# Kernel optimization log

Measured on AMD Instinct MI355X. Metric: run time of the kernel, lower is better.

The kernel has to match this reference:

```python
import jax, jax.numpy as jnp
import numpy as np

K = 20
EPS = 1e-5   # BatchNorm eps (eval mode: running_mean=0, running_var=1)
SLOPE = 0.2


def knn_idx(x, k):
    # x: [B,F,N] -> idx [B,N,k]; top-k of negative squared distance (includes self)
    xx = jnp.sum(x * x, axis=1)                       # [B,N]
    inner = jnp.einsum('bfn,bfm->bnm', x, x)          # [B,N,N]
    neg_d = 2.0 * inner - xx[:, :, None] - xx[:, None, :]
    _, idx = jax.lax.top_k(neg_d, k)
    return idx


def gather_neighbors(x_nt, idx):
    # x_nt [B,N,F], idx [B,N,k] -> [B,N,k,F]
    return jax.vmap(lambda xt, ix: xt[ix])(x_nt, idx)


def group_layer(x_bfn, idx):
    # GroupLayer: [B,F,N] -> [B,2F,N,k] = cat(neigh - center, neigh)
    x_nt = jnp.transpose(x_bfn, (0, 2, 1))
    neigh = gather_neighbors(x_nt, idx)
    feat = jnp.concatenate([neigh - x_nt[:, :, None, :], neigh], axis=-1)
    return jnp.transpose(feat, (0, 3, 1, 2))


def eigen_graph(pts_bfn, k):
    # pts_bfn [B,3,N] -> feature [B,15,N], idx_EU [B,N,k], idx_EI [B,N,k]
    B, _, N = pts_bfn.shape
    idx_eu = knn_idx(pts_bfn, k)
    pts_nt = jnp.transpose(pts_bfn, (0, 2, 1))        # [B,N,3]
    neigh = gather_neighbors(pts_nt, idx_eu)          # [B,N,k,3]
    diff = neigh - pts_nt[:, :, None, :]
    cov = jnp.einsum('bnki,bnkj->bnij', diff, diff)   # [B,N,3,3] symmetric PSD
    eigval, eigvec = jnp.linalg.eigh(cov)             # [B,N,3], [B,N,3,3]
    feature = jnp.concatenate([pts_nt, eigval, eigvec.reshape(B, N, 9)], axis=2)
    idx_ei = knn_idx(jnp.transpose(eigval, (0, 2, 1)), k)
    return jnp.transpose(feature, (0, 2, 1)), idx_eu, idx_ei


def first_group_layer(x_bfn, idx_eu, idx_ei):
    # x_bfn [B,15,N]: [:,0:3]=xyz, [:,3:6]=eigenvalues -> [B,12,N,k]
    xyz = jnp.transpose(x_bfn[:, 0:3, :], (0, 2, 1))
    eig = jnp.transpose(x_bfn[:, 3:6, :], (0, 2, 1))
    nx = gather_neighbors(xyz, idx_eu)
    gx = jnp.concatenate([nx - xyz[:, :, None, :], nx], axis=-1)
    ne = gather_neighbors(eig, idx_ei)
    ge = jnp.concatenate([ne - eig[:, :, None, :], ne], axis=-1)
    out = jnp.concatenate([gx, ge], axis=-1)
    return jnp.transpose(out, (0, 3, 1, 2))


def graph_distance(pts_bfn, idx):
    pts_nt = jnp.transpose(pts_bfn, (0, 2, 1))
    d = gather_neighbors(pts_nt, idx) - pts_nt[:, :, None, :]
    s = jnp.sum(d * d, axis=-1)
    return jnp.sqrt(jnp.maximum(s, 1e-12))[:, None, :, :]  # [B,1,N,k]


def conv_bn_lrelu(x, w, g, b):
    # 1x1 conv (no bias) + eval-mode BN + LeakyReLU(0.2)
    if x.ndim == 4:
        y = jnp.einsum('oc,bcnk->bonk', w, x)
        g_, b_ = g[None, :, None, None], b[None, :, None, None]
    else:
        y = jnp.einsum('oc,bcn->bon', w, x)
        g_, b_ = g[None, :, None], b[None, :, None]
    y = y / jnp.sqrt(1.0 + EPS) * g_ + b_
    return jax.nn.leaky_relu(y, SLOPE)


def fps(points, n_samples):
    # furthest point sampling, start at index 0. points [B,N,3] -> [B,S] int32
    B, N, _ = points.shape
    init = jnp.zeros((B,), jnp.int32)
    dist0 = jnp.full((B, N), 1e10, points.dtype)

    def body(carry, _):
        dist, last = carry
        lastp = jnp.take_along_axis(points, last[:, None, None].astype(jnp.int32), axis=1)
        d = jnp.sum((points - lastp) ** 2, axis=-1)
        dist = jnp.minimum(dist, d)
        nxt = jnp.argmax(dist, axis=-1).astype(jnp.int32)
        return (dist, nxt), nxt

    (_, _), rest = jax.lax.scan(body, (dist0, init), None, length=n_samples - 1)
    return jnp.concatenate([init[None, :], rest], axis=0).T


def gather_op(x_bcn, idx):
    # x [B,C,N], idx [B,S] -> [B,C,S]
    return jnp.take_along_axis(x_bcn, idx[:, None, :], axis=2)


def forward(x, conv1_w, bn1_g, bn1_b, conv2_w, bn2_g, bn2_b, conv3_w, bn3_g, bn3_b,
            conv5_w, bn5_g, bn5_b, lin1_w, bn6_g, bn6_b, lin2_w, lin2_b,
            bn7_g, bn7_b, lin3_w, lin3_b):
    B, _, N1 = x.shape
    N2, N3 = N1 // 2, N1 // 4
    pts1 = jnp.transpose(x, (0, 2, 1))  # [B,N,3]

    # GSCM layer 1 (first layer)
    feat, idx_eu, idx_ei = eigen_graph(x, K)
    g = first_group_layer(feat, idx_eu, idx_ei)            # [B,12,N1,K]
    g = jnp.concatenate([g, graph_distance(x, idx_eu)], axis=1)  # [B,13,N1,K]
    x1 = conv_bn_lrelu(g, conv1_w, bn1_g, bn1_b).max(axis=-1)     # [B,64,N1]

    # downsample to N2
    id2 = fps(pts1, N2)
    pts2_bfn = gather_op(x, id2)                            # [B,3,N2]
    x1_ds = gather_op(x1, id2)                              # [B,64,N2]

    # GSCM layer 2
    _, idx_eu2, idx_ei2 = eigen_graph(pts2_bfn, K)
    g2 = jnp.concatenate([group_layer(x1_ds, idx_eu2), group_layer(x1_ds, idx_ei2)], axis=1)
    x2 = conv_bn_lrelu(g2, conv2_w, bn2_g, bn2_b).max(axis=-1)    # [B,64,N2]

    # downsample to N3
    pts2_nt = jnp.transpose(pts2_bfn, (0, 2, 1))
    id3 = fps(pts2_nt, N3)
    pts3_bfn = gather_op(pts2_bfn, id3)
    x2_ds = gather_op(x2, id3)
    x1_ds = gather_op(x1_ds, id3)

    # GSCM layer 3
    _, idx_eu3, idx_ei3 = eigen_graph(pts3_bfn, K)
    g3 = jnp.concatenate([group_layer(x2_ds, idx_eu3), group_layer(x2_ds, idx_ei3)], axis=1)
    x3 = conv_bn_lrelu(g3, conv3_w, bn3_g, bn3_b).max(axis=-1)    # [B,128,N3]

    h = jnp.concatenate([x1_ds, x2_ds, x3], axis=1)        # [B,256,N3]
    h = conv_bn_lrelu(h, conv5_w, bn5_g, bn5_b)            # [B,emb,N3]
    h = jnp.concatenate([h.max(axis=-1), h.mean(axis=-1)], axis=1)  # [B,2*emb]

    y = jnp.einsum('oi,bi->bo', lin1_w, h)
    y = jax.nn.leaky_relu(y / jnp.sqrt(1.0 + EPS) * bn6_g + bn6_b, SLOPE)
    y = jnp.einsum('oi,bi->bo', lin2_w, y) + lin2_b
    y = jax.nn.leaky_relu(y / jnp.sqrt(1.0 + EPS) * bn7_g + bn7_b, SLOPE)
    return jnp.einsum('oi,bi->bo', lin3_w, y) + lin3_b     # [B,40]


def setup_inputs() -> dict:
    key = jax.random.key(0)
    ks = jax.random.split(key, 10)
    B, N, EMB, OUT = 16, 1024, 1024, 40

    def w(k_, o, i):
        return jax.random.normal(k_, (o, i), jnp.float32) * (1.0 / np.sqrt(i))

    return {
        'x': jax.random.normal(ks[0], (B, 3, N), jnp.float32),
        'conv1_w': w(ks[1], 64, 13), 'bn1_g': jnp.ones((64,)), 'bn1_b': jnp.zeros((64,)),
        'conv2_w': w(ks[2], 64, 256), 'bn2_g': jnp.ones((64,)), 'bn2_b': jnp.zeros((64,)),
        'conv3_w': w(ks[3], 128, 256), 'bn3_g': jnp.ones((128,)), 'bn3_b': jnp.zeros((128,)),
        'conv5_w': w(ks[4], EMB, 256), 'bn5_g': jnp.ones((EMB,)), 'bn5_b': jnp.zeros((EMB,)),
        'lin1_w': w(ks[5], 512, 2 * EMB), 'bn6_g': jnp.ones((512,)), 'bn6_b': jnp.zeros((512,)),
        'lin2_w': w(ks[6], 256, 512), 'lin2_b': jnp.zeros((256,)),
        'bn7_g': jnp.ones((256,)), 'bn7_b': jnp.zeros((256,)),
        'lin3_w': w(ks[7], OUT, 256), 'lin3_b': jnp.zeros((OUT,)),
    }


def reference(x, conv1_w, bn1_g, bn1_b, conv2_w, bn2_g, bn2_b, conv3_w, bn3_g, bn3_b,
              conv5_w, bn5_g, bn5_b, lin1_w, bn6_g, bn6_b, lin2_w, lin2_b,
              bn7_g, bn7_b, lin3_w, lin3_b):
    return forward(x, conv1_w, bn1_g, bn1_b, conv2_w, bn2_g, bn2_b, conv3_w, bn3_g, bn3_b,
                   conv5_w, bn5_g, bn5_b, lin1_w, bn6_g, bn6_b, lin2_w, lin2_b,
                   bn7_g, bn7_b, lin3_w, lin3_b)
```

## Files before the change

### kernel.cpp

```cpp
#include <hip/hip_runtime.h>
#include <math.h>

#define KNB 20
constexpr float BN_INV = 0.9999950000374997f;
constexpr float SLOPE = 0.2f;

__device__ __forceinline__ float lrelu(float v){ return v >= 0.f ? v : SLOPE*v; }

__global__ __launch_bounds__(256) void prep_kernel(const float* __restrict__ x, float* __restrict__ pts,
                            const float* __restrict__ conv2w, float* __restrict__ Wc2,
                            const float* __restrict__ conv3w, float* __restrict__ Wc3){
  int i = blockIdx.x*256 + threadIdx.x;
  if (i < 16*1024){
    int b = i >> 10, n = i & 1023;
    const float* xb = x + (size_t)b*3*1024;
    float* p = pts + (size_t)i*3;
    p[0]=xb[n]; p[1]=xb[1024+n]; p[2]=xb[2048+n];
  } else if (i < 16*1024 + 64*64){
    int e = i - 16*1024;
    int o = e >> 6, c = e & 63;
    float wa=conv2w[(size_t)o*256+c], wb=conv2w[(size_t)o*256+64+c];
    float wc=conv2w[(size_t)o*256+128+c], wd=conv2w[(size_t)o*256+192+c];
    Wc2[((size_t)0*64+o)*64+c]=wa+wb; Wc2[((size_t)1*64+o)*64+c]=wc+wd; Wc2[((size_t)2*64+o)*64+c]=wa+wc;
  } else if (i < 16*1024 + 64*64 + 128*64){
    int e = i - 16*1024 - 64*64;
    int o = e >> 6, c = e & 63;
    float wa=conv3w[(size_t)o*256+c], wb=conv3w[(size_t)o*256+64+c];
    float wc=conv3w[(size_t)o*256+128+c], wd=conv3w[(size_t)o*256+192+c];
    Wc3[((size_t)0*128+o)*64+c]=wa+wb; Wc3[((size_t)1*128+o)*64+c]=wc+wd; Wc3[((size_t)2*128+o)*64+c]=wa+wc;
  }
}

template<int N, bool TOGLOBAL>
__device__ void knn_core(const float* __restrict__ pts, int* __restrict__ idx_global,
                         int* __restrict__ sOut, int chunk, int b, float4* sp){
#pragma clang fp contract(off)
  constexpr int E = N/64;
  int t = threadIdx.x;
  const float* pb = pts + (size_t)b*N*3;
  for (int e = t; e < N; e += 256){
    float x0=pb[e*3], x1=pb[e*3+1], x2=pb[e*3+2];
    sp[e] = make_float4(x0, x1, x2, (x0*x0 + x1*x1) + x2*x2);
  }
  __syncthreads();
  int wave = t >> 6, lane = t & 63;
  int row = chunk*4 + wave;
  float4 P = sp[row];
  float nd[E];
  #pragma unroll
  for (int i=0;i<E;++i){
    float4 Q = sp[lane + i*64];
    float inner = (P.x*Q.x + P.y*Q.y) + P.z*Q.z;
    nd[i] = (2.0f*inner - P.w) - Q.w;
  }
  int myout = 0;
  for (int j=0;j<KNB;++j){
    float bv = nd[0]; int bi = lane;
    #pragma unroll
    for (int i=1;i<E;++i){
      if (nd[i] > bv){ bv = nd[i]; bi = lane + i*64; }
    }
    #pragma unroll
    for (int off=1; off<64; off<<=1){
      float ov = __shfl_xor(bv, off);
      int oi = __shfl_xor(bi, off);
      if (ov > bv || (ov == bv && oi < bi)){ bv = ov; bi = oi; }
    }
    if (lane == j) myout = bi;
    if (lane == (bi & 63)){
      int slot = bi >> 6;
      #pragma unroll
      for (int i=0;i<E;++i) if (i == slot) nd[i] = -INFINITY;
    }
  }
  if (TOGLOBAL){
    if (lane < KNB) idx_global[((size_t)b*N + row)*KNB + lane] = myout;
  } else {
    if (lane < KNB) sOut[lane] = myout;
  }
}

template<int N>
__global__ __launch_bounds__(256) void knn_kernel(const float* __restrict__ pts, int* __restrict__ idx){
  __shared__ float4 sp[N];
  knn_core<N,true>(pts, idx, nullptr, blockIdx.x, blockIdx.y, sp);
}

#define DECLQ4(i) float4 Q##i = sp[(i)*256 + tid]; float D##i = 1e10f; \
  asm volatile("" : "+v"(Q##i.x), "+v"(Q##i.y), "+v"(Q##i.z));
#define UPD4(i, B) { float dx=Q##i.x-L.x; float dy=Q##i.y-L.y; float dz=Q##i.z-L.z; \
  float dd=fminf(D##i,(dx*dx+dy*dy)+dz*dz); D##i=dd; \
  unsigned long long k=((unsigned long long)__float_as_uint(dd)<<32)|(unsigned long long)(nl-(unsigned)((i)*256)); \
  if(k>B)B=k; }
#define DPPMAX(ctrl) { unsigned lo=(unsigned)bk, hi=(unsigned)(bk>>32); \
  unsigned lo2=(unsigned)__builtin_amdgcn_mov_dpp((int)lo, ctrl, 0xF, 0xF, true); \
  unsigned hi2=(unsigned)__builtin_amdgcn_mov_dpp((int)hi, ctrl, 0xF, 0xF, true); \
  unsigned long long ok=((unsigned long long)hi2<<32)|lo2; if(ok>bk)bk=ok; }
#define FPS_STEP_TAIL \
      DPPMAX(0xB1) DPPMAX(0x4E) DPPMAX(0x124) DPPMAX(0x128) DPPMAX(0x142) DPPMAX(0x143) \
      if (lane == 63) rk[((s&1)<<2) | w] = bk; \
      __syncthreads(); \
      { const unsigned long long* rp = rk + ((s&1)<<2); \
        unsigned long long k0=rp[0], k1=rp[1], k2=rp[2], k3=rp[3]; \
        unsigned long long km1 = k0>k1?k0:k1, km2 = k2>k3?k2:k3; \
        unsigned long long kk = km1>km2?km1:km2; \
        last = (int)(~(unsigned int)kk); } \
      if (tid==0) idout[(size_t)b*M + s] = last;

template<int N, int M>
__device__ void fps_body4(const float* __restrict__ pts, int* __restrict__ idout,
                          int b, float4* sp, unsigned long long* rk){
#pragma clang fp contract(off)
  constexpr int E4 = N/256;
  int tid = threadIdx.x;
  const float* pb = pts + (size_t)b*N*3;
  for (int e=tid; e<N; e+=256){
    sp[e] = make_float4(pb[e*3], pb[e*3+1], pb[e*3+2], 0.f);
  }
  __syncthreads();
  __builtin_amdgcn_s_setprio(1);
  int lane = tid & 63, w = tid >> 6;
  unsigned int nl = ~(unsigned int)tid;
  int last = 0;
  if (tid==0) idout[(size_t)b*M] = 0;
  if constexpr (E4 == 4){
    DECLQ4(0) DECLQ4(1) DECLQ4(2) DECLQ4(3)
    for (int s=1; s<M; ++s){
      float4 L = sp[last];
      unsigned long long b0=0ULL,b1=0ULL,b2=0ULL,b3=0ULL;
      UPD4(0,b0) UPD4(1,b1) UPD4(2,b2) UPD4(3,b3)
      unsigned long long kl_ = b0>b1?b0:b1, kh_ = b2>b3?b2:b3;
      unsigned long long bk = kl_>kh_?kl_:kh_;
      FPS_STEP_TAIL
    }
  } else {
    DECLQ4(0) DECLQ4(1)
    for (int s=1; s<M; ++s){
      float4 L = sp[last];
      unsigned long long b0=0ULL,b1=0ULL;
      UPD4(0,b0) UPD4(1,b1)
      unsigned long long bk = b0>b1?b0:b1;
      FPS_STEP_TAIL
    }
  }
}

template<int N>
__global__ void cov_eig_kernel(const float* __restrict__ pts, const int* __restrict__ idx,
                               float* __restrict__ eigval){
  int i = blockIdx.x*blockDim.x + threadIdx.x;
  if (i >= 16*N) return;
  int b = i / N, n = i % N;
  const float* pb = pts + (size_t)b*N*3;
  const int* ix = idx + (size_t)i*KNB;
  float cx = pb[n*3], cy = pb[n*3+1], cz = pb[n*3+2];
  float c00=0,c01=0,c02=0,c11=0,c12=0,c22=0;
  for (int k=0;k<KNB;++k){
    int m = ix[k];
    float dx = pb[m*3]-cx, dy = pb[m*3+1]-cy, dz = pb[m*3+2]-cz;
    c00 += dx*dx; c01 += dx*dy; c02 += dx*dz;
    c11 += dy*dy; c12 += dy*dz; c22 += dz*dz;
  }
  double a00=c00,a01=c01,a02=c02,a11=c11,a12=c12,a22=c22;
  double p1 = a01*a01 + a02*a02 + a12*a12;
  double q = (a00+a11+a22)/3.0;
  double b00=a00-q, b11=a11-q, b22=a22-q;
  double p2 = b00*b00+b11*b11+b22*b22 + 2.0*p1;
  double e0,e1,e2;
  if (p2 <= 0.0){
    e0=e1=e2=q;
  } else {
    double p = sqrt(p2/6.0);
    double det = b00*(b11*b22 - a12*a12) - a01*(a01*b22 - a12*a02) + a02*(a01*a12 - b11*a02);
    double r = det / (2.0*p*p*p);
    r = fmin(1.0, fmax(-1.0, r));
    double phi = acos(r)/3.0;
    double big = q + 2.0*p*cos(phi);
    double sml = q + 2.0*p*cos(phi + 2.0943951023931953);
    double mid = 3.0*q - big - sml;
    e0 = sml; e1 = mid; e2 = big;
  }
  float* ev = eigval + (size_t)i*3;
  ev[0]=(float)e0; ev[1]=(float)e1; ev[2]=(float)e2;
}

__device__ void stage1_body(
    const float* __restrict__ eig, const float* __restrict__ pts,
    const int* __restrict__ idx_eu,
    const float* __restrict__ w, const float* __restrict__ g, const float* __restrict__ bb,
    float* __restrict__ x1, int chunk, int b,
    float4* sp, int (*sIei)[KNB], float (*feat)[13][KNB]){
  constexpr int N = 1024;
  int t = threadIdx.x, wave = t>>6, lane = t&63;
  knn_core<N,false>(eig, nullptr, &sIei[wave][0], chunk, b, sp);
  int row = chunk*4 + wave;
  size_t i = (size_t)b*N + row;
  const float* pb = pts + (size_t)b*N*3;
  if (lane < KNB){
    int ieu = idx_eu[i*KNB + lane];
    int iei = sIei[wave][lane];
    float4 ne4 = sp[iei];
    float4 ee4 = sp[row];
    float d2 = 0.f;
    #pragma unroll
    for (int f=0; f<3; ++f){
      float nx = pb[ieu*3+f], xx = pb[row*3+f];
      float dfv = nx - xx;
      feat[wave][f][lane] = dfv; feat[wave][3+f][lane] = nx;
      float ne = (f==0)? ne4.x : ((f==1)? ne4.y : ne4.z);
      float ee = (f==0)? ee4.x : ((f==1)? ee4.y : ee4.z);
      feat[wave][6+f][lane] = ne - ee; feat[wave][9+f][lane] = ne;
      d2 += dfv*dfv;
    }
    feat[wave][12][lane] = sqrtf(fmaxf(d2, 1e-12f));
  }
  __syncthreads();
  float wr[13];
  #pragma unroll
  for (int c=0;c<13;++c) wr[c] = w[lane*13+c];
  float sg = BN_INV * g[lane], sb = bb[lane];
  float mx = -INFINITY;
  for (int k=0;k<KNB;++k){
    float s = 0.f;
    #pragma unroll
    for (int c=0;c<13;++c) s = fmaf(wr[c], feat[wave][c][k], s);
    mx = fmaxf(mx, lrelu(fmaf(s, sg, sb)));
  }
  x1[i*64 + lane] = mx;
}

__global__ __launch_bounds__(256, 1) void mega1_kernel(
    const float* __restrict__ pts1, int* __restrict__ fps_id,
    const float* __restrict__ eig1, const int* __restrict__ idx_eu,
    const float* __restrict__ w, const float* __restrict__ g, const float* __restrict__ bb,
    float* __restrict__ x1){
  __shared__ float4 sp[1024];
  __shared__ int sIei[4][KNB];
  __shared__ float feat[4][13][KNB];
  __shared__ unsigned long long rk[8];
  if (blockIdx.x < 16){
    fps_body4<1024,512>(pts1, fps_id, blockIdx.x, sp, rk);
  } else {
    int bx = blockIdx.x - 16;
    stage1_body(eig1, pts1, idx_eu, w, g, bb, x1, bx & 255, bx >> 8, sp, sIei, feat);
  }
}

template<int COUT, int N>
__device__ void gm_body(const float* __restrict__ eig,
    const float* __restrict__ PQR, int Mtot,
    const int* __restrict__ idx_eu,
    const float* __restrict__ g, const float* __restrict__ bb,
    float* __restrict__ xout, int chunk, int b, float4* sp, int* sIeiW){
  int t = threadIdx.x, wave = t>>6, lane = t&63;
  knn_core<N,false>(eig, nullptr, sIeiW, chunk, b, sp);
  __syncthreads();
  int row = chunk*4 + wave;
  size_t i = (size_t)b*N + row;
  const float* P = PQR;
  const float* Q = PQR + (size_t)Mtot*COUT;
  const float* R = PQR + (size_t)2*Mtot*COUT;
  for (int o = lane; o < COUT; o += 64){
    float base = R[i*COUT + o];
    float sg = BN_INV*g[o], sb = bb[o];
    float mx = -INFINITY;
    for (int k=0;k<KNB;++k){
      int eu = idx_eu[i*KNB + k];
      int ei = sIeiW[k];
      float v = P[((size_t)b*N + eu)*COUT + o] + Q[((size_t)b*N + ei)*COUT + o] - base;
      mx = fmaxf(mx, lrelu(fmaf(v, sg, sb)));
    }
    xout[i*COUT + o] = mx;
  }
}

template<int COUT, int N>
__global__ __launch_bounds__(256) void knn_ei_gm_kernel(
    const float* __restrict__ eig, const float* __restrict__ PQR, int Mtot,
    const int* __restrict__ idx_eu, const float* __restrict__ g, const float* __restrict__ bb,
    float* __restrict__ xout){
  __shared__ float4 sp[N];
  __shared__ int sIei[4][KNB];
  int wave = threadIdx.x >> 6;
  gm_body<COUT,N>(eig, PQR, Mtot, idx_eu, g, bb, xout, blockIdx.x, blockIdx.y, sp, &sIei[wave][0]);
}

template<int COUT, int N, int M>
__global__ __launch_bounds__(256, 1) void gmfps_kernel(
    const float* __restrict__ eig, const float* __restrict__ ptsN,
    const float* __restrict__ PQR, int Mtot,
    const int* __restrict__ idx_eu, const float* __restrict__ g, const float* __restrict__ bb,
    float* __restrict__ xout, int* __restrict__ fps_id){
  __shared__ float4 sp[N];
  __shared__ int sIei[4][KNB];
  __shared__ unsigned long long rk[8];
  if (blockIdx.x < 16){
    fps_body4<N,M>(ptsN, fps_id, blockIdx.x, sp, rk);
    return;
  }
  int bx = blockIdx.x - 16;
  int wave = threadIdx.x >> 6;
  gm_body<COUT,N>(eig, PQR, Mtot, idx_eu, g, bb, xout, bx % (N/4), bx / (N/4), sp, &sIei[wave][0]);
}

__global__ __launch_bounds__(256) void gather2_kernel(const float* __restrict__ pts1, const float* __restrict__ x1,
                               const int* __restrict__ id2, float* __restrict__ pts2, float* __restrict__ x1d){
  int i = blockIdx.x*256 + threadIdx.x;
  if (i < 16*512){
    int b = i >> 9;
    int src = id2[i];
    const float* p = pts1 + ((size_t)b*1024 + src)*3;
    float* o = pts2 + (size_t)i*3;
    o[0]=p[0]; o[1]=p[1]; o[2]=p[2];
  } else {
    int e = i - 16*512;
    if (e < 16*512*64){
      int c = e & 63, r = e >> 6;
      int b = r >> 9, s = r & 511;
      int src = id2[(size_t)b*512 + s];
      x1d[e] = x1[((size_t)b*1024 + src)*64 + c];
    }
  }
}

__global__ __launch_bounds__(256) void gather3_kernel(const float* __restrict__ pts2, const float* __restrict__ x2,
                               const float* __restrict__ x1d, const int* __restrict__ id3,
                               float* __restrict__ pts3, float* __restrict__ x2d, float* __restrict__ x1dd){
  int i = blockIdx.x*256 + threadIdx.x;
  if (i < 16*256){
    int b = i >> 8;
    int src = id3[i];
    const float* p = pts2 + ((size_t)b*512 + src)*3;
    float* o = pts3 + (size_t)i*3;
    o[0]=p[0]; o[1]=p[1]; o[2]=p[2];
  } else {
    int e = i - 16*256;
    if (e < 16*256*64){
      int c = e & 63, r = e >> 6;
      int b = r >> 8, s = r & 255;
      int src = id3[(size_t)b*256 + s];
      x2d[e] = x2[((size_t)b*512 + src)*64 + c];
    } else {
      int e2 = e - 16*256*64;
      if (e2 < 16*256*64){
        int c = e2 & 63, r = e2 >> 6;
        int b = r >> 8, s = r & 255;
        int src = id3[(size_t)b*256 + s];
        x1dd[e2] = x1d[((size_t)b*512 + src)*64 + c];
      }
    }
  }
}

template<int COUT>
__global__ __launch_bounds__(256) void gemm_xw_kernel(
    const float* __restrict__ X, const float* __restrict__ Wc,
    float* __restrict__ PQR, int Mtot){
  __shared__ float sA[64][68];
  __shared__ float sW[64][68];
  int mt = blockIdx.x, ot = blockIdx.y, set = blockIdx.z;
  int t = threadIdx.x;
  for (int e=t; e<4096; e+=256){ int r=e>>6, c=e&63; sA[r][c] = X[(size_t)(mt*64+r)*64 + c]; }
  const float* Wp = Wc + ((size_t)set*COUT + ot*64)*64;
  for (int e=t; e<4096; e+=256){ int r=e>>6, c=e&63; sW[r][c] = Wp[(size_t)r*64 + c]; }
  __syncthreads();
  int tx = t & 15, ty = t >> 4;
  float acc[4][4];
  #pragma unroll
  for (int r=0;r<4;++r)
    #pragma unroll
    for (int j=0;j<4;++j) acc[r][j]=0.f;
  #pragma unroll
  for (int k4=0;k4<16;++k4){
    float4 A0 = *(const float4*)&sA[ty*4+0][k4*4];
    float4 A1 = *(const float4*)&sA[ty*4+1][k4*4];
    float4 A2 = *(const float4*)&sA[ty*4+2][k4*4];
    float4 A3 = *(const float4*)&sA[ty*4+3][k4*4];
    float4 W0 = *(const float4*)&sW[tx*4+0][k4*4];
    float4 W1 = *(const float4*)&sW[tx*4+1][k4*4];
    float4 W2 = *(const float4*)&sW[tx*4+2][k4*4];
    float4 W3 = *(const float4*)&sW[tx*4+3][k4*4];
    float4 A[4] = {A0,A1,A2,A3};
    float4 W[4] = {W0,W1,W2,W3};
    #pragma unroll
    for (int r=0;r<4;++r)
      #pragma unroll
      for (int j=0;j<4;++j){
        float s = acc[r][j];
        s = fmaf(A[r].x, W[j].x, s);
        s = fmaf(A[r].y, W[j].y, s);
        s = fmaf(A[r].z, W[j].z, s);
        s = fmaf(A[r].w, W[j].w, s);
        acc[r][j] = s;
      }
  }
  float* outp = PQR + (size_t)set*Mtot*COUT;
  #pragma unroll
  for (int r=0;r<4;++r){
    float4 v = make_float4(acc[r][0], acc[r][1], acc[r][2], acc[r][3]);
    *(float4*)&outp[(size_t)(mt*64 + ty*4 + r)*COUT + ot*64 + tx*4] = v;
  }
}

__global__ __launch_bounds__(256) void conv5_gemm_kernel(
    const float* __restrict__ x1dd, const float* __restrict__ x2d, const float* __restrict__ x3,
    const float* __restrict__ w, const float* __restrict__ g, const float* __restrict__ bb,
    float* __restrict__ pmax, float* __restrict__ psum){
  __shared__ float sA[64][68];
  __shared__ float sB[64][68];
  int otile = blockIdx.x, ntile = blockIdx.y, b = blockIdx.z;
  int t = threadIdx.x;
  int tx = t & 15, ty = t >> 4;
  float acc[4][4];
  #pragma unroll
  for (int i=0;i<4;++i)
    #pragma unroll
    for (int j=0;j<4;++j) acc[i][j] = 0.f;
  for (int kc=0; kc<4; ++kc){
    #pragma unroll 4
    for (int e = t; e < 4096; e += 256){
      int nl = e >> 6, kl = e & 63;
      int n = ntile*64 + nl;
      float v;
      if (kc == 0)      v = x1dd[((size_t)b*256 + n)*64 + kl];
      else if (kc == 1) v = x2d [((size_t)b*256 + n)*64 + kl];
      else              v = x3  [((size_t)b*256 + n)*128 + (kc-2)*64 + kl];
      sA[nl][kl] = v;
    }
    #pragma unroll 4
    for (int e = t; e < 4096; e += 256){
      int ol = e >> 6, kl = e & 63;
      sB[ol][kl] = w[((size_t)(otile*64 + ol))*256 + kc*64 + kl];
    }
    __syncthreads();
    #pragma unroll
    for (int k4=0; k4<16; ++k4){
      float4 a0 = *(const float4*)&sA[ty*4+0][k4*4];
      float4 a1 = *(const float4*)&sA[ty*4+1][k4*4];
      float4 a2 = *(const float4*)&sA[ty*4+2][k4*4];
      float4 a3 = *(const float4*)&sA[ty*4+3][k4*4];
      float4 b0 = *(const float4*)&sB[tx*4+0][k4*4];
      float4 b1 = *(const float4*)&sB[tx*4+1][k4*4];
      float4 b2 = *(const float4*)&sB[tx*4+2][k4*4];
      float4 b3 = *(const float4*)&sB[tx*4+3][k4*4];
      float4 A[4] = {a0,a1,a2,a3};
      float4 Bv[4] = {b0,b1,b2,b3};
      #pragma unroll
      for (int i=0;i<4;++i)
        #pragma unroll
        for (int j=0;j<4;++j){
          float s = acc[i][j];
          s = fmaf(A[i].x, Bv[j].x, s);
          s = fmaf(A[i].y, Bv[j].y, s);
          s = fmaf(A[i].z, Bv[j].z, s);
          s = fmaf(A[i].w, Bv[j].w, s);
          acc[i][j] = s;
        }
    }
    __syncthreads();
  }
  float sg[4], sbv[4];
  #pragma unroll
  for (int j=0;j<4;++j){
    int o = otile*64 + tx*4 + j;
    sg[j] = BN_INV*g[o]; sbv[j] = bb[o];
  }
  float mx[4], sm[4];
  #pragma unroll
  for (int j=0;j<4;++j){ mx[j]=-INFINITY; sm[j]=0.f; }
  #pragma unroll
  for (int i=0;i<4;++i)
    #pragma unroll
    for (int j=0;j<4;++j){
      float vv = lrelu(fmaf(acc[i][j], sg[j], sbv[j]));
      mx[j] = fmaxf(mx[j], vv);
      sm[j] += vv;
    }
  float* redM = &sA[0][0];
  float* redS = redM + 16*64;
  #pragma unroll
  for (int j=0;j<4;++j){
    redM[ty*64 + tx*4 + j] = mx[j];
    redS[ty*64 + tx*4 + j] = sm[j];
  }
  __syncthreads();
  if (t < 64){
    float m = -INFINITY, s = 0.f;
    #pragma unroll
    for (int r=0;r<16;++r){
      m = fmaxf(m, redM[r*64 + t]);
      s += redS[r*64 + t];
    }
    int o = otile*64 + t;
    pmax[((size_t)b*1024 + o)*4 + ntile] = m;
    psum[((size_t)b*1024 + o)*4 + ntile] = s;
  }
}

__global__ __launch_bounds__(256) void lin1_kernel(const float* __restrict__ pmax, const float* __restrict__ psum,
    const float* __restrict__ w, const float* __restrict__ g, const float* __restrict__ bb,
    float* __restrict__ y1){
  __shared__ float sh[2048];
  int b = blockIdx.y; int o = blockIdx.x*256 + threadIdx.x;
  for (int e=threadIdx.x; e<2048; e+=256){
    if (e < 1024){
      const float* pm = pmax + ((size_t)b*1024 + e)*4;
      sh[e] = fmaxf(fmaxf(pm[0],pm[1]), fmaxf(pm[2],pm[3]));
    } else {
      const float* ps = psum + ((size_t)b*1024 + (e-1024))*4;
      sh[e] = ((ps[0]+ps[1])+(ps[2]+ps[3])) * (1.0f/256.0f);
    }
  }
  __syncthreads();
  const float* wr = w + (size_t)o*2048;
  float acc=0.f;
  for (int c=0;c<2048;++c) acc = fmaf(wr[c], sh[c], acc);
  y1[(size_t)b*512+o] = lrelu(fmaf(acc, BN_INV*g[o], bb[o]));
}

__global__ __launch_bounds__(256) void lin23_kernel(const float* __restrict__ y1,
    const float* __restrict__ w2, const float* __restrict__ lb2,
    const float* __restrict__ g, const float* __restrict__ bb,
    const float* __restrict__ w3, const float* __restrict__ lb3,
    float* __restrict__ outp){
  __shared__ float sh1[512];
  __shared__ float sh2[256];
  int b = blockIdx.x; int o = threadIdx.x;
  for (int e=o; e<512; e+=256) sh1[e]=y1[(size_t)b*512+e];
  __syncthreads();
  {
    const float* wr = w2 + (size_t)o*512;
    float acc=0.f;
    for (int c=0;c<512;++c) acc = fmaf(wr[c], sh1[c], acc);
    acc += lb2[o];
    sh2[o] = lrelu(fmaf(acc, BN_INV*g[o], bb[o]));
  }
  __syncthreads();
  if (o < 40){
    const float* wr = w3 + (size_t)o*256;
    float acc=0.f;
    for (int c=0;c<256;++c) acc = fmaf(wr[c], sh2[c], acc);
    outp[(size_t)b*40+o] = acc + lb3[o];
  }
}

extern "C" void kernel_launch(void* const* d_in, const int* in_sizes, int n_in,
                              void* d_out, int out_size, void* d_ws, size_t ws_size,
                              hipStream_t stream) {
  const float* x      = (const float*)d_in[0];
  const float* conv1w = (const float*)d_in[1];
  const float* bn1g   = (const float*)d_in[2];
  const float* bn1b   = (const float*)d_in[3];
  const float* conv2w = (const float*)d_in[4];
  const float* bn2g   = (const float*)d_in[5];
  const float* bn2b   = (const float*)d_in[6];
  const float* conv3w = (const float*)d_in[7];
  const float* bn3g   = (const float*)d_in[8];
  const float* bn3b   = (const float*)d_in[9];
  const float* conv5w = (const float*)d_in[10];
  const float* bn5g   = (const float*)d_in[11];
  const float* bn5b   = (const float*)d_in[12];
  const float* lin1w  = (const float*)d_in[13];
  const float* bn6g   = (const float*)d_in[14];
  const float* bn6b   = (const float*)d_in[15];
  const float* lin2w  = (const float*)d_in[16];
  const float* lin2b  = (const float*)d_in[17];
  const float* bn7g   = (const float*)d_in[18];
  const float* bn7b   = (const float*)d_in[19];
  const float* lin3w  = (const float*)d_in[20];
  const float* lin3b  = (const float*)d_in[21];
  float* outp = (float*)d_out;

  char* ws = (char*)d_ws;
  size_t off = 0;
  auto alloc = [&](size_t bytes)->char*{
    off = (off + 255) & ~(size_t)255;
    char* p = ws + off; off += bytes; return p;
  };
  const int B=16, N1=1024, N2=512, N3=256;
  float* pts1 = (float*)alloc((size_t)B*N1*3*4);
  int*   ieu1 = (int*)alloc((size_t)B*N1*KNB*4);
  float* eig1 = (float*)alloc((size_t)B*N1*3*4);
  float* x1   = (float*)alloc((size_t)B*N1*64*4);
  int*   id2  = (int*)alloc((size_t)B*N2*4);
  float* pts2 = (float*)alloc((size_t)B*N2*3*4);
  float* x1d  = (float*)alloc((size_t)B*N2*64*4);
  int*   ieu2 = (int*)alloc((size_t)B*N2*KNB*4);
  float* eig2 = (float*)alloc((size_t)B*N2*3*4);
  float* x2   = (float*)alloc((size_t)B*N2*64*4);
  int*   id3  = (int*)alloc((size_t)B*N3*4);
  float* pts3 = (float*)alloc((size_t)B*N3*3*4);
  float* x2d  = (float*)alloc((size_t)B*N3*64*4);
  float* x1dd = (float*)alloc((size_t)B*N3*64*4);
  int*   ieu3 = (int*)alloc((size_t)B*N3*KNB*4);
  float* eig3 = (float*)alloc((size_t)B*N3*3*4);
  float* x3   = (float*)alloc((size_t)B*N3*128*4);
  float* pmax = (float*)alloc((size_t)B*1024*4*4);
  float* psum = (float*)alloc((size_t)B*1024*4*4);
  float* y1   = (float*)alloc((size_t)B*512*4);
  float* Wc2  = (float*)alloc((size_t)3*64*64*4);
  float* Wc3  = (float*)alloc((size_t)3*128*64*4);
  float* PQR2 = (float*)alloc((size_t)3*B*N2*64*4);
  float* PQR3 = (float*)alloc((size_t)3*B*N3*128*4);

  prep_kernel<<<112, 256, 0, stream>>>(x, pts1, conv2w, Wc2, conv3w, Wc3);
  knn_kernel<1024><<<dim3(256,16), 256, 0, stream>>>(pts1, ieu1);
  cov_eig_kernel<1024><<<(B*N1+255)/256, 256, 0, stream>>>(pts1, ieu1, eig1);
  mega1_kernel<<<16 + 4096, 256, 0, stream>>>(pts1, id2, eig1, ieu1, conv1w, bn1g, bn1b, x1);
  gather2_kernel<<<2080, 256, 0, stream>>>(pts1, x1, id2, pts2, x1d);
  knn_kernel<512><<<dim3(128,16), 256, 0, stream>>>(pts2, ieu2);
  cov_eig_kernel<512><<<(B*N2+255)/256, 256, 0, stream>>>(pts2, ieu2, eig2);
  gemm_xw_kernel<64><<<dim3(B*N2/64, 1, 3), 256, 0, stream>>>(x1d, Wc2, PQR2, B*N2);
  gmfps_kernel<64,512,256><<<16 + 2048, 256, 0, stream>>>(eig2, pts2, PQR2, B*N2, ieu2, bn2g, bn2b, x2, id3);
  gather3_kernel<<<2064, 256, 0, stream>>>(pts2, x2, x1d, id3, pts3, x2d, x1dd);
  knn_kernel<256><<<dim3(64,16), 256, 0, stream>>>(pts3, ieu3);
  cov_eig_kernel<256><<<(B*N3+255)/256, 256, 0, stream>>>(pts3, ieu3, eig3);
  gemm_xw_kernel<128><<<dim3(B*N3/64, 2, 3), 256, 0, stream>>>(x2d, Wc3, PQR3, B*N3);
  knn_ei_gm_kernel<128,256><<<dim3(64,16), 256, 0, stream>>>(eig3, PQR3, B*N3, ieu3, bn3g, bn3b, x3);
  conv5_gemm_kernel<<<dim3(16,4,16), 256, 0, stream>>>(x1dd, x2d, x3, conv5w, bn5g, bn5b, pmax, psum);
  lin1_kernel<<<dim3(2,16), 256, 0, stream>>>(pmax, psum, lin1w, bn6g, bn6b, y1);
  lin23_kernel<<<16, 256, 0, stream>>>(y1, lin2w, lin2b, bn7g, bn7b, lin3w, lin3b, outp);
}
```

Baseline: 602.1 us.

## Fuse kNN with covariance eigen solve and merge independent GEMM launches

Merges the kNN and covariance-eigenvalue kernels: each block now handles several rows per wave, keeps the indices in shared memory and computes eigenvalues from the shared point cache, so the index re-read and one launch go away. At stages 2 and 3 the independent X·W GEMM blocks are folded into the same launch as the kNN/cov blocks, cutting launches and letting the two workloads run side by side. The costs are more rows per block and higher shared-memory use, since both GEMM tiles and the point cache are allocated in every block, which can lower occupancy. The eigen step now runs on only 4×RPW threads per block, which serialises it.

```diff
diff --git a/kernel.cpp b/kernel.cpp
--- a/kernel.cpp
+++ b/kernel.cpp
@@ -31,11 +31,44 @@
   }
 }
 
+template<int N>
+__device__ int knn_row(const float4* sp, int row, int lane){
+#pragma clang fp contract(off)
+  constexpr int E = N/64;
+  float4 P = sp[row];
+  float nd[E];
+  #pragma unroll
+  for (int i=0;i<E;++i){
+    float4 Q = sp[lane + i*64];
+    float inner = (P.x*Q.x + P.y*Q.y) + P.z*Q.z;
+    nd[i] = (2.0f*inner - P.w) - Q.w;
+  }
+  int myout = 0;
+  for (int j=0;j<KNB;++j){
+    float bv = nd[0]; int bi = lane;
+    #pragma unroll
+    for (int i=1;i<E;++i){
+      if (nd[i] > bv){ bv = nd[i]; bi = lane + i*64; }
+    }
+    #pragma unroll
+    for (int off=1; off<64; off<<=1){
+      float ov = __shfl_xor(bv, off);
+      int oi = __shfl_xor(bi, off);
+      if (ov > bv || (ov == bv && oi < bi)){ bv = ov; bi = oi; }
+    }
+    if (lane == j) myout = bi;
+    if (lane == (bi & 63)){
+      int slot = bi >> 6;
+      #pragma unroll
+      for (int i=0;i<E;++i) if (i == slot) nd[i] = -INFINITY;
+    }
+  }
+  return myout;
+}
+
 template<int N, bool TOGLOBAL>
 __device__ void knn_core(const float* __restrict__ pts, int* __restrict__ idx_global,
                          int* __restrict__ sOut, int chunk, int b, float4* sp){
-#pragma clang fp contract(off)
-  constexpr int E = N/64;
   int t = threadIdx.x;
   const float* pb = pts + (size_t)b*N*3;
   for (int e = t; e < N; e += 256){
@@ -45,34 +78,7 @@
   __syncthreads();
   int wave = t >> 6, lane = t & 63;
   int row = chunk*4 + wave;
-  float4 P = sp[row];
-  float nd[E];
-  #pragma unroll
-  for (int i=0;i<E;++i){
-    float4 Q = sp[lane + i*64];
-    float inner = (P.x*Q.x + P.y*Q.y) + P.z*Q.z;
-    nd[i] = (2.0f*inner - P.w) - Q.w;
-  }
-  int myout = 0;
-  for (int j=0;j<KNB;++j){
-    float bv = nd[0]; int bi = lane;
-    #pragma unroll
-    for (int i=1;i<E;++i){
-      if (nd[i] > bv){ bv = nd[i]; bi = lane + i*64; }
-    }
-    #pragma unroll
-    for (int off=1; off<64; off<<=1){
-      float ov = __shfl_xor(bv, off);
-      int oi = __shfl_xor(bi, off);
-      if (ov > bv || (ov == bv && oi < bi)){ bv = ov; bi = oi; }
-    }
-    if (lane == j) myout = bi;
-    if (lane == (bi & 63)){
-      int slot = bi >> 6;
-      #pragma unroll
-      for (int i=0;i<E;++i) if (i == slot) nd[i] = -INFINITY;
-    }
-  }
+  int myout = knn_row<N>(sp, row, lane);
   if (TOGLOBAL){
     if (lane < KNB) idx_global[((size_t)b*N + row)*KNB + lane] = myout;
   } else {
@@ -80,10 +86,73 @@
   }
 }
 
-template<int N>
-__global__ __launch_bounds__(256) void knn_kernel(const float* __restrict__ pts, int* __restrict__ idx){
+__device__ void cov_eig_row(const float4* sp, const int* sIdxRow, int row, float* ev){
+  float cx = sp[row].x, cy = sp[row].y, cz = sp[row].z;
+  float c00=0,c01=0,c02=0,c11=0,c12=0,c22=0;
+  for (int k=0;k<KNB;++k){
+    int m = sIdxRow[k];
+    float dx = sp[m].x-cx, dy = sp[m].y-cy, dz = sp[m].z-cz;
+    c00 += dx*dx; c01 += dx*dy; c02 += dx*dz;
+    c11 += dy*dy; c12 += dy*dz; c22 += dz*dz;
+  }
+  double a00=c00,a01=c01,a02=c02,a11=c11,a12=c12,a22=c22;
+  double p1 = a01*a01 + a02*a02 + a12*a12;
+  double q = (a00+a11+a22)/3.0;
+  double b00=a00-q, b11=a11-q, b22=a22-q;
+  double p2 = b00*b00+b11*b11+b22*b22 + 2.0*p1;
+  double e0,e1,e2;
+  if (p2 <= 0.0){
+    e0=e1=e2=q;
+  } else {
+    double p = sqrt(p2/6.0);
+    double det = b00*(b11*b22 - a12*a12) - a01*(a01*b22 - a12*a02) + a02*(a01*a12 - b11*a02);
+    double r = det / (2.0*p*p*p);
+    r = fmin(1.0, fmax(-1.0, r));
+    double phi = acos(r)/3.0;
+    double big = q + 2.0*p*cos(phi);
+    double sml = q + 2.0*p*cos(phi + 2.0943951023931953);
+    double mid = 3.0*q - big - sml;
+    e0 = sml; e1 = mid; e2 = big;
+  }
+  ev[0]=(float)e0; ev[1]=(float)e1; ev[2]=(float)e2;
+}
+
+template<int N, int RPW>
+__device__ void knn_cov_body(const float* __restrict__ pts, int* __restrict__ idx,
+                             float* __restrict__ eigval, int cb, int b,
+                             float4* sp, int (*sIdx)[KNB]){
+  constexpr int ROWS = 4*RPW;
+  int t = threadIdx.x;
+  const float* pb = pts + (size_t)b*N*3;
+  for (int e = t; e < N; e += 256){
+    float x0=pb[e*3], x1=pb[e*3+1], x2=pb[e*3+2];
+    sp[e] = make_float4(x0, x1, x2, (x0*x0 + x1*x1) + x2*x2);
+  }
+  __syncthreads();
+  int wave = t >> 6, lane = t & 63;
+  #pragma unroll
+  for (int r=0; r<RPW; ++r){
+    int lr = wave*RPW + r;
+    int row = cb*ROWS + lr;
+    int myout = knn_row<N>(sp, row, lane);
+    if (lane < KNB){
+      sIdx[lr][lane] = myout;
+      idx[((size_t)b*N + row)*KNB + lane] = myout;
+    }
+  }
+  __syncthreads();
+  if (t < ROWS){
+    int row = cb*ROWS + t;
+    cov_eig_row(sp, &sIdx[t][0], row, eigval + ((size_t)b*N + row)*3);
+  }
+}
+
+template<int N, int RPW>
+__global__ __launch_bounds__(256) void knn_cov_kernel(const float* __restrict__ pts,
+    int* __restrict__ idx, float* __restrict__ eigval){
   __shared__ float4 sp[N];
-  knn_core<N,true>(pts, idx, nullptr, blockIdx.x, blockIdx.y, sp);
+  __shared__ int sIdx[4*RPW][KNB];
+  knn_cov_body<N,RPW>(pts, idx, eigval, blockIdx.x, blockIdx.y, sp, sIdx);
 }
 
 #define DECLQ4(i) float4 Q##i = sp[(i)*256 + tid]; float D##i = 1e10f; \
@@ -145,45 +214,6 @@
   }
 }
 
-template<int N>
-__global__ void cov_eig_kernel(const float* __restrict__ pts, const int* __restrict__ idx,
-                               float* __restrict__ eigval){
-  int i = blockIdx.x*blockDim.x + threadIdx.x;
-  if (i >= 16*N) return;
-  int b = i / N, n = i % N;
-  const float* pb = pts + (size_t)b*N*3;
-  const int* ix = idx + (size_t)i*KNB;
-  float cx = pb[n*3], cy = pb[n*3+1], cz = pb[n*3+2];
-  float c00=0,c01=0,c02=0,c11=0,c12=0,c22=0;
-  for (int k=0;k<KNB;++k){
-    int m = ix[k];
-    float dx = pb[m*3]-cx, dy = pb[m*3+1]-cy, dz = pb[m*3+2]-cz;
-    c00 += dx*dx; c01 += dx*dy; c02 += dx*dz;
-    c11 += dy*dy; c12 += dy*dz; c22 += dz*dz;
-  }
-  double a00=c00,a01=c01,a02=c02,a11=c11,a12=c12,a22=c22;
-  double p1 = a01*a01 + a02*a02 + a12*a12;
-  double q = (a00+a11+a22)/3.0;
-  double b00=a00-q, b11=a11-q, b22=a22-q;
-  double p2 = b00*b00+b11*b11+b22*b22 + 2.0*p1;
-  double e0,e1,e2;
-  if (p2 <= 0.0){
-    e0=e1=e2=q;
-  } else {
-    double p = sqrt(p2/6.0);
-    double det = b00*(b11*b22 - a12*a12) - a01*(a01*b22 - a12*a02) + a02*(a01*a12 - b11*a02);
-    double r = det / (2.0*p*p*p);
-    r = fmin(1.0, fmax(-1.0, r));
-    double phi = acos(r)/3.0;
-    double big = q + 2.0*p*cos(phi);
-    double sml = q + 2.0*p*cos(phi + 2.0943951023931953);
-    double mid = 3.0*q - big - sml;
-    e0 = sml; e1 = mid; e2 = big;
-  }
-  float* ev = eigval + (size_t)i*3;
-  ev[0]=(float)e0; ev[1]=(float)e1; ev[2]=(float)e2;
-}
-
 __device__ void stage1_body(
     const float* __restrict__ eig, const float* __restrict__ pts,
     const int* __restrict__ idx_eu,
@@ -303,6 +333,86 @@
   gm_body<COUT,N>(eig, PQR, Mtot, idx_eu, g, bb, xout, bx % (N/4), bx / (N/4), sp, &sIei[wave][0]);
 }
 
+template<int COUT>
+__device__ void gemm_xw_body(const float* __restrict__ X, const float* __restrict__ Wc,
+    float* __restrict__ PQR, int Mtot, int mt, int ot, int set,
+    float (*sA)[68], float (*sW)[68]){
+  int t = threadIdx.x;
+  for (int e=t; e<4096; e+=256){ int r=e>>6, c=e&63; sA[r][c] = X[(size_t)(mt*64+r)*64 + c]; }
+  const float* Wp = Wc + ((size_t)set*COUT + ot*64)*64;
+  for (int e=t; e<4096; e+=256){ int r=e>>6, c=e&63; sW[r][c] = Wp[(size_t)r*64 + c]; }
+  __syncthreads();
+  int tx = t & 15, ty = t >> 4;
+  float acc[4][4];
+  #pragma unroll
+  for (int r=0;r<4;++r)
+    #pragma unroll
+    for (int j=0;j<4;++j) acc[r][j]=0.f;
+  #pragma unroll
+  for (int k4=0;k4<16;++k4){
+    float4 A0 = *(const float4*)&sA[ty*4+0][k4*4];
+    float4 A1 = *(const float4*)&sA[ty*4+1][k4*4];
+    float4 A2 = *(const float4*)&sA[ty*4+2][k4*4];
+    float4 A3 = *(const float4*)&sA[ty*4+3][k4*4];
+    float4 W0 = *(const float4*)&sW[tx*4+0][k4*4];
+    float4 W1 = *(const float4*)&sW[tx*4+1][k4*4];
+    float4 W2 = *(const float4*)&sW[tx*4+2][k4*4];
+    float4 W3 = *(const float4*)&sW[tx*4+3][k4*4];
+    float4 A[4] = {A0,A1,A2,A3};
+    float4 W[4] = {W0,W1,W2,W3};
+    #pragma unroll
+    for (int r=0;r<4;++r)
+      #pragma unroll
+      for (int j=0;j<4;++j){
+        float s = acc[r][j];
+        s = fmaf(A[r].x, W[j].x, s);
+        s = fmaf(A[r].y, W[j].y, s);
+        s = fmaf(A[r].z, W[j].z, s);
+        s = fmaf(A[r].w, W[j].w, s);
+        acc[r][j] = s;
+      }
+  }
+  float* outp = PQR + (size_t)set*Mtot*COUT;
+  #pragma unroll
+  for (int r=0;r<4;++r){
+    float4 v = make_float4(acc[r][0], acc[r][1], acc[r][2], acc[r][3]);
+    *(float4*)&outp[(size_t)(mt*64 + ty*4 + r)*COUT + ot*64 + tx*4] = v;
+  }
+}
+
+__global__ __launch_bounds__(256) void a2_kernel(
+    const float* __restrict__ pts2, int* __restrict__ ieu2, float* __restrict__ eig2,
+    const float* __restrict__ x1d, const float* __restrict__ Wc2, float* __restrict__ PQR2){
+  __shared__ float4 sp[512];
+  __shared__ int sIdx[8][KNB];
+  __shared__ float sA[64][68];
+  __shared__ float sW[64][68];
+  int bx = blockIdx.x;
+  if (bx < 1024){
+    knn_cov_body<512,2>(pts2, ieu2, eig2, bx & 63, bx >> 6, sp, sIdx);
+  } else {
+    int b2 = bx - 1024;
+    gemm_xw_body<64>(x1d, Wc2, PQR2, 16*512, b2 & 127, 0, b2 >> 7, sA, sW);
+  }
+}
+
+__global__ __launch_bounds__(256) void a3_kernel(
+    const float* __restrict__ pts3, int* __restrict__ ieu3, float* __restrict__ eig3,
+    const float* __restrict__ x2d, const float* __restrict__ Wc3, float* __restrict__ PQR3){
+  __shared__ float4 sp[256];
+  __shared__ int sIdx[4][KNB];
+  __shared__ float sA[64][68];
+  __shared__ float sW[64][68];
+  int bx = blockIdx.x;
+  if (bx < 1024){
+    knn_cov_body<256,1>(pts3, ieu3, eig3, bx & 63, bx >> 6, sp, sIdx);
+  } else {
+    int b2 = bx - 1024;
+    int mt = b2 & 63, rest = b2 >> 6;
+    gemm_xw_body<128>(x2d, Wc3, PQR3, 16*256, mt, rest & 1, rest >> 1, sA, sW);
+  }
+}
+
 __global__ __launch_bounds__(256) void gather2_kernel(const float* __restrict__ pts1, const float* __restrict__ x1,
                                const int* __restrict__ id2, float* __restrict__ pts2, float* __restrict__ x1d){
   int i = blockIdx.x*256 + threadIdx.x;
@@ -349,56 +459,6 @@
         x1dd[e2] = x1d[((size_t)b*512 + src)*64 + c];
       }
     }
-  }
-}
-
-template<int COUT>
-__global__ __launch_bounds__(256) void gemm_xw_kernel(
-    const float* __restrict__ X, const float* __restrict__ Wc,
-    float* __restrict__ PQR, int Mtot){
-  __shared__ float sA[64][68];
-  __shared__ float sW[64][68];
-  int mt = blockIdx.x, ot = blockIdx.y, set = blockIdx.z;
-  int t = threadIdx.x;
-  for (int e=t; e<4096; e+=256){ int r=e>>6, c=e&63; sA[r][c] = X[(size_t)(mt*64+r)*64 + c]; }
-  const float* Wp = Wc + ((size_t)set*COUT + ot*64)*64;
-  for (int e=t; e<4096; e+=256){ int r=e>>6, c=e&63; sW[r][c] = Wp[(size_t)r*64 + c]; }
-  __syncthreads();
-  int tx = t & 15, ty = t >> 4;
-  float acc[4][4];
-  #pragma unroll
-  for (int r=0;r<4;++r)
-    #pragma unroll
-    for (int j=0;j<4;++j) acc[r][j]=0.f;
-  #pragma unroll
-  for (int k4=0;k4<16;++k4){
-    float4 A0 = *(const float4*)&sA[ty*4+0][k4*4];
-    float4 A1 = *(const float4*)&sA[ty*4+1][k4*4];
-    float4 A2 = *(const float4*)&sA[ty*4+2][k4*4];
-    float4 A3 = *(const float4*)&sA[ty*4+3][k4*4];
-    float4 W0 = *(const float4*)&sW[tx*4+0][k4*4];
-    float4 W1 = *(const float4*)&sW[tx*4+1][k4*4];
-    float4 W2 = *(const float4*)&sW[tx*4+2][k4*4];
-    float4 W3 = *(const float4*)&sW[tx*4+3][k4*4];
-    float4 A[4] = {A0,A1,A2,A3};
-    float4 W[4] = {W0,W1,W2,W3};
-    #pragma unroll
-    for (int r=0;r<4;++r)
-      #pragma unroll
-      for (int j=0;j<4;++j){
-        float s = acc[r][j];
-        s = fmaf(A[r].x, W[j].x, s);
-        s = fmaf(A[r].y, W[j].y, s);
-        s = fmaf(A[r].z, W[j].z, s);
-        s = fmaf(A[r].w, W[j].w, s);
-        acc[r][j] = s;
-      }
-  }
-  float* outp = PQR + (size_t)set*Mtot*COUT;
-  #pragma unroll
-  for (int r=0;r<4;++r){
-    float4 v = make_float4(acc[r][0], acc[r][1], acc[r][2], acc[r][3]);
-    *(float4*)&outp[(size_t)(mt*64 + ty*4 + r)*COUT + ot*64 + tx*4] = v;
   }
 }
 
@@ -604,18 +664,13 @@
   float* PQR3 = (float*)alloc((size_t)3*B*N3*128*4);
 
   prep_kernel<<<112, 256, 0, stream>>>(x, pts1, conv2w, Wc2, conv3w, Wc3);
-  knn_kernel<1024><<<dim3(256,16), 256, 0, stream>>>(pts1, ieu1);
-  cov_eig_kernel<1024><<<(B*N1+255)/256, 256, 0, stream>>>(pts1, ieu1, eig1);
+  knn_cov_kernel<1024,4><<<dim3(64,16), 256, 0, stream>>>(pts1, ieu1, eig1);
   mega1_kernel<<<16 + 4096, 256, 0, stream>>>(pts1, id2, eig1, ieu1, conv1w, bn1g, bn1b, x1);
   gather2_kernel<<<2080, 256, 0, stream>>>(pts1, x1, id2, pts2, x1d);
-  knn_kernel<512><<<dim3(128,16), 256, 0, stream>>>(pts2, ieu2);
-  cov_eig_kernel<512><<<(B*N2+255)/256, 256, 0, stream>>>(pts2, ieu2, eig2);
-  gemm_xw_kernel<64><<<dim3(B*N2/64, 1, 3), 256, 0, stream>>>(x1d, Wc2, PQR2, B*N2);
+  a2_kernel<<<1024 + 384, 256, 0, stream>>>(pts2, ieu2, eig2, x1d, Wc2, PQR2);
   gmfps_kernel<64,512,256><<<16 + 2048, 256, 0, stream>>>(eig2, pts2, PQR2, B*N2, ieu2, bn2g, bn2b, x2, id3);
   gather3_kernel<<<2064, 256, 0, stream>>>(pts2, x2, x1d, id3, pts3, x2d, x1dd);
-  knn_kernel<256><<<dim3(64,16), 256, 0, stream>>>(pts3, ieu3);
-  cov_eig_kernel<256><<<(B*N3+255)/256, 256, 0, stream>>>(pts3, ieu3, eig3);
-  gemm_xw_kernel<128><<<dim3(B*N3/64, 2, 3), 256, 0, stream>>>(x2d, Wc3, PQR3, B*N3);
+  a3_kernel<<<1024 + 384, 256, 0, stream>>>(pts3, ieu3, eig3, x2d, Wc3, PQR3);
   knn_ei_gm_kernel<128,256><<<dim3(64,16), 256, 0, stream>>>(eig3, PQR3, B*N3, ieu3, bn3g, bn3b, x3);
   conv5_gemm_kernel<<<dim3(16,4,16), 256, 0, stream>>>(x1dd, x2d, x3, conv5w, bn5g, bn5b, pmax, psum);
   lin1_kernel<<<dim3(2,16), 256, 0, stream>>>(pmax, psum, lin1w, bn6g, bn6b, y1);
```

New measurement: 628.1 us. +4.3%, slower.
